# Kernel optimization log

Hardware: AMD Instinct MI355X
Metric: run time of the kernel (lower is better)

Reference implementation:

```python
import jax, jax.numpy as jnp
import numpy as np
import math

B, S, D, H = 4, 2048, 1024, 16
HD = D // H  # head_dim = 64


def _rope_tables(max_len, half_dim, theta=10000.0):
    inv_freq = 1.0 / (theta ** (jnp.arange(0, half_dim, dtype=jnp.float32) / half_dim))
    ang = jnp.arange(max_len, dtype=jnp.float32)[:, None] * inv_freq[None, :]  # [max_len, half_dim]
    return jnp.cos(ang), jnp.sin(ang)


def _apply_rope(x, cos, sin):
    # x: [B, H, S, HD]; cos/sin: [S, HD/2]
    x1, x2 = x[..., ::2], x[..., 1::2]
    # matches torch.cat([x1*cos - x2*sin, x1*sin + x2*cos], dim=-1)
    return jnp.concatenate([x1 * cos - x2 * sin, x1 * sin + x2 * cos], axis=-1)


def setup_inputs() -> dict:
    key = jax.random.key(0)
    kx, kq, ko = jax.random.split(key, 3)
    x = jax.random.normal(kx, (B, S, D), dtype=jnp.float32)
    Wqkv = jax.random.normal(kq, (D, 3 * D), dtype=jnp.float32) / math.sqrt(D)
    Wout = jax.random.normal(ko, (D, D), dtype=jnp.float32) / math.sqrt(D)
    cos, sin = _rope_tables(S, HD // 2)
    # causal additive mask, per-batch as in module signature [B, S, S]
    causal = jnp.where(jnp.tril(jnp.ones((S, S), dtype=bool)), 0.0, -1e9).astype(jnp.float32)
    mask = jnp.broadcast_to(causal, (B, S, S))
    return {"x": x, "cos": cos, "sin": sin, "mask": mask, "Wqkv": Wqkv, "Wout": Wout}


def reference(x, cos, sin, mask, Wqkv, Wout):
    b, s, d = x.shape
    qkv = x @ Wqkv  # [B, S, 3D]
    q, k, v = jnp.split(qkv, 3, axis=-1)
    def to_heads(t):
        return t.reshape(b, s, H, HD).transpose(0, 2, 1, 3)  # [B, H, S, HD]
    q, k, v = to_heads(q), to_heads(k), to_heads(v)
    q = _apply_rope(q, cos[:s], sin[:s])
    k = _apply_rope(k, cos[:s], sin[:s])
    scores = jnp.einsum("bhqd,bhkd->bhqk", q, k) / math.sqrt(HD)
    attn = jax.nn.softmax(scores + mask[:, None, :, :], axis=-1)
    out = jnp.einsum("bhqk,bhkd->bhqd", attn, v)  # [B, H, S, HD]
    out = out.transpose(0, 2, 1, 3).reshape(b, s, d)
    return out @ Wout
```

## Files before the change

### kernel.cpp

```cpp
#include <hip/hip_runtime.h>
#include <hip/hip_bf16.h>
#include <stdint.h>

#define B_   4
#define S_   2048
#define D_   1024
#define H_   16
#define HD_  64
#define BH_  (B_*H_)
#define MROWS (B_*S_)

typedef short  short8  __attribute__((ext_vector_type(8)));
typedef float  floatx4 __attribute__((ext_vector_type(4)));

__device__ __forceinline__ ushort f2bf(float f) {
    union { float f; uint32_t u; } v; v.f = f;
    uint32_t u = v.u;
    return (ushort)((u + 0x7FFFu + ((u >> 16) & 1u)) >> 16);
}
__device__ __forceinline__ float u2f(uint32_t u) {
    union { uint32_t u; float f; } v; v.u = u; return v.f;
}
__device__ __forceinline__ uint32_t f2u(float f) {
    union { float f; uint32_t u; } v; v.f = f; return v.u;
}

__device__ __forceinline__ void gl_lds16(const ushort* g, ushort* l) {
    __builtin_amdgcn_global_load_lds(
        (const __attribute__((address_space(1))) unsigned int*)g,
        (__attribute__((address_space(3))) unsigned int*)l,
        16, 0, 0);
}

__global__ void k_f32_to_bf16(const float* __restrict__ in, ushort* __restrict__ out, int n) {
    int i = (blockIdx.x * blockDim.x + threadIdx.x) * 4;
    if (i + 3 < n) {
        float4 f = *(const float4*)(in + i);
        ushort4 o; o.x = f2bf(f.x); o.y = f2bf(f.y); o.z = f2bf(f.z); o.w = f2bf(f.w);
        *(ushort4*)(out + i) = o;
    }
}

__global__ void k_transpose_to_bf16(const float* __restrict__ in, ushort* __restrict__ out,
                                    int R, int C) {
    __shared__ float tile[32][33];
    int bx = blockIdx.x * 32;
    int by = blockIdx.y * 32;
    int tx = threadIdx.x;
    int ty = threadIdx.y;
    #pragma unroll
    for (int j = 0; j < 32; j += 8)
        tile[ty + j][tx] = in[(size_t)(by + ty + j) * C + bx + tx];
    __syncthreads();
    #pragma unroll
    for (int j = 0; j < 32; j += 8)
        out[(size_t)(bx + ty + j) * R + by + tx] = f2bf(tile[tx][ty + j]);
}

__global__ void k_vtrans(const ushort* __restrict__ Vb, ushort* __restrict__ VbT) {
    __shared__ __align__(16) ushort t[64 * 72];
    int bh = blockIdx.x >> 5;
    int s0 = (blockIdx.x & 31) * 64;
    int tid = threadIdx.x;
    int ss = tid >> 2, c0 = (tid & 3) * 16;
    size_t base = (size_t)bh * S_ * HD_;
    *(uint4*)&t[ss * 72 + c0]     = *(const uint4*)&Vb[base + (size_t)(s0 + ss) * HD_ + c0];
    *(uint4*)&t[ss * 72 + c0 + 8] = *(const uint4*)&Vb[base + (size_t)(s0 + ss) * HD_ + c0 + 8];
    __syncthreads();
    int hd = tid >> 2, q0 = (tid & 3) * 16;
    ushort tmp[16];
    #pragma unroll
    for (int e = 0; e < 16; e++) tmp[e] = t[(q0 + e) * 72 + hd];
    size_t obase = (size_t)bh * HD_ * S_ + (size_t)hd * S_ + s0 + q0;
    *(uint4*)&VbT[obase]     = *(const uint4*)&tmp[0];
    *(uint4*)&VbT[obase + 8] = *(const uint4*)&tmp[8];
}

#define BM 128
#define BN 128
#define BK 64

template<int EPI>
__global__ __launch_bounds__(256)
void k_gemm(const ushort* __restrict__ A, const ushort* __restrict__ Bt,
            float* __restrict__ outF,
            ushort* __restrict__ q_out, ushort* __restrict__ k_out, ushort* __restrict__ v_out,
            int M, int N, int K) {
    __shared__ __align__(16) ushort As[BM * 64];
    __shared__ __align__(16) ushort Bs[BN * 64];
    int tid  = threadIdx.x;
    int lane = tid & 63;
    int wave = tid >> 6;
    int quad = lane >> 4;
    int l16  = lane & 15;
    int bm = blockIdx.y * BM;
    int bn = blockIdx.x * BN;
    int wm = (wave >> 1) * 64;
    int wn = (wave & 1) * 64;

    floatx4 acc[4][4] = {};

    for (int k0 = 0; k0 < K; k0 += BK) {
        __syncthreads();
        #pragma unroll
        for (int i = 0; i < 4; i++) {
            int c   = i * 256 + tid;
            int row = c >> 3;
            int gc  = (c & 7) ^ (row & 7);
            gl_lds16(&A[(size_t)(bm + row) * K + k0 + gc * 8],  &As[c * 8]);
            gl_lds16(&Bt[(size_t)(bn + row) * K + k0 + gc * 8], &Bs[c * 8]);
        }
        __syncthreads();
        #pragma unroll
        for (int kk = 0; kk < 2; kk++) {
            short8 af[4], bf[4];
            #pragma unroll
            for (int mt = 0; mt < 4; mt++)
                af[mt] = *(const short8*)&As[(wm + mt * 16 + l16) * 64 +
                                             (((kk * 4 + quad) ^ (l16 & 7)) << 3)];
            #pragma unroll
            for (int nt = 0; nt < 4; nt++)
                bf[nt] = *(const short8*)&Bs[(wn + nt * 16 + l16) * 64 +
                                             (((kk * 4 + quad) ^ (l16 & 7)) << 3)];
            #pragma unroll
            for (int mt = 0; mt < 4; mt++)
                #pragma unroll
                for (int nt = 0; nt < 4; nt++)
                    acc[mt][nt] = __builtin_amdgcn_mfma_f32_16x16x32_bf16(af[mt], bf[nt], acc[mt][nt], 0, 0, 0);
        }
    }

    #pragma unroll
    for (int mt = 0; mt < 4; mt++)
        #pragma unroll
        for (int nt = 0; nt < 4; nt++)
            #pragma unroll
            for (int r = 0; r < 4; r++) {
                int row = bm + wm + mt * 16 + quad * 4 + r;
                int col = bn + wn + nt * 16 + l16;
                float v = acc[mt][nt][r];
                if (EPI == 0) {
                    int which = col >> 10;
                    int rem   = col & 1023;
                    int h  = rem >> 6, hd = rem & 63;
                    int b  = row >> 11, s  = row & 2047;
                    size_t idx = ((size_t)(b * H_ + h) * S_ + s) * HD_ + hd;
                    ushort bv = f2bf(v);
                    ushort* dst = (which == 0) ? q_out : (which == 1) ? k_out : v_out;
                    dst[idx] = bv;
                } else {
                    outF[(size_t)row * N + col] = v;
                }
            }
}

__global__ void k_rope(ushort* __restrict__ Q, ushort* __restrict__ Kv,
                       const float* __restrict__ cosT, const float* __restrict__ sinT) {
    int wid  = (blockIdx.x * 256 + threadIdx.x) >> 6;
    int lane = threadIdx.x & 63;
    int s  = wid & (S_ - 1);
    int bh = wid >> 11;
    int i  = lane & 31;
    float c  = cosT[s * 32 + i];
    float sn = sinT[s * 32 + i];
    size_t base = ((size_t)bh * S_ + s) * HD_;

    uint32_t uq = *(const uint32_t*)&Q[base + 2 * i];
    float x1 = u2f(uq << 16), x2 = u2f(uq & 0xFFFF0000u);
    float o  = (lane < 32) ? (x1 * c - x2 * sn) : (x1 * sn + x2 * c);
    Q[base + lane] = f2bf(o * 0.1803368801f);

    uint32_t uk = *(const uint32_t*)&Kv[base + 2 * i];
    x1 = u2f(uk << 16); x2 = u2f(uk & 0xFFFF0000u);
    o  = (lane < 32) ? (x1 * c - x2 * sn) : (x1 * sn + x2 * c);
    Kv[base + lane] = f2bf(o);
}

__global__ __launch_bounds__(256, 4)
void k_attn(const ushort* __restrict__ Q, const ushort* __restrict__ K,
            const ushort* __restrict__ VT, ushort* __restrict__ O) {
    __shared__ __align__(16) ushort Ks[64 * 64];
    __shared__ __align__(16) ushort Vt[64 * 64];
    __shared__ __align__(16) ushort Pst[4][32 * 64];

    int tid  = threadIdx.x;
    int lane = tid & 63;
    int wave = tid >> 6;
    int quad = lane >> 4;
    int l16  = lane & 15;

    int bh   = blockIdx.x & 63;
    int qblk = 15 - (blockIdx.x >> 6);
    int qb0  = qblk * 128;
    size_t hbase = (size_t)bh * S_ * HD_;
    size_t vbase = (size_t)bh * HD_ * S_;

    int mrow[2] = { qb0 + wave * 16, qb0 + 64 + wave * 16 };

    short8 qf[2][2];
    #pragma unroll
    for (int m = 0; m < 2; m++)
        #pragma unroll
        for (int h = 0; h < 2; h++)
            qf[m][h] = *(const short8*)&Q[hbase + (size_t)(mrow[m] + l16) * HD_ + quad * 8 + h * 32];

    short8 ones;
    #pragma unroll
    for (int e = 0; e < 8; e++) ones[e] = (short)0x3F80;

    floatx4 acc[2][4] = {};
    floatx4 accl[2] = {};

    int nk = 2 * qblk + 2;
    for (int kb = 0; kb < nk; kb++) {
        int k0 = kb * 64;
        __syncthreads();
        #pragma unroll
        for (int i = 0; i < 2; i++) {
            int c   = i * 256 + tid;
            int row = c >> 3;
            int gc  = (c & 7) ^ (row & 7);
            gl_lds16(&K[hbase + (size_t)(k0 + row) * HD_ + gc * 8], &Ks[c * 8]);
            gl_lds16(&VT[vbase + (size_t)row * S_ + k0 + gc * 8],   &Vt[c * 8]);
        }
        __syncthreads();

        bool act[2] = { k0 <= mrow[0] + 15, k0 <= mrow[1] + 15 };

        #pragma unroll
        for (int m = 0; m < 2; m++) {
            if (!act[m]) continue;
            floatx4 sc[4] = {};
            #pragma unroll
            for (int kt = 0; kt < 4; kt++)
                #pragma unroll
                for (int h = 0; h < 2; h++) {
                    short8 kf = *(const short8*)&Ks[(kt * 16 + l16) * 64 +
                                                    (((h * 4 + quad) ^ (l16 & 7)) << 3)];
                    sc[kt] = __builtin_amdgcn_mfma_f32_16x16x32_bf16(kf, qf[m][h], sc[kt], 0, 0, 0);
                }
            bool needMask = (k0 + 63 > mrow[m]);
            int qr = mrow[m] + l16;
            #pragma unroll
            for (int kt = 0; kt < 4; kt++) {
                float p[4];
                #pragma unroll
                for (int r = 0; r < 4; r++) {
                    float v = exp2f(sc[kt][r]);
                    if (needMask) {
                        int kc = k0 + kt * 16 + quad * 4 + r;
                        if (kc > qr) v = 0.0f;
                    }
                    p[r] = v;
                }
                uint2 pk;
                pk.x = __builtin_amdgcn_perm(f2u(p[1]) + 0x8000u, f2u(p[0]) + 0x8000u, 0x07060302u);
                pk.y = __builtin_amdgcn_perm(f2u(p[3]) + 0x8000u, f2u(p[2]) + 0x8000u, 0x07060302u);
                int pc = (kt * 4 + quad) ^ (l16 & 14);
                *(uint2*)&Pst[wave][(m * 16 + l16) * 64 + pc * 4] = pk;
            }
        }

        #pragma unroll
        for (int k2 = 0; k2 < 2; k2++) {
            short8 vb[4];
            #pragma unroll
            for (int nt = 0; nt < 4; nt++)
                vb[nt] = *(const short8*)&Vt[(nt * 16 + l16) * 64 +
                                             (((k2 * 4 + quad) ^ (l16 & 7)) << 3)];
            #pragma unroll
            for (int m = 0; m < 2; m++) {
                if (!act[m]) continue;
                int pe = (k2 * 8 + quad * 2) ^ (l16 & 14);
                short8 pa = *(const short8*)&Pst[wave][(m * 16 + l16) * 64 + pe * 4];
                #pragma unroll
                for (int nt = 0; nt < 4; nt++)
                    acc[m][nt] = __builtin_amdgcn_mfma_f32_16x16x32_bf16(pa, vb[nt], acc[m][nt], 0, 0, 0);
                accl[m] = __builtin_amdgcn_mfma_f32_16x16x32_bf16(pa, ones, accl[m], 0, 0, 0);
            }
        }
    }

    int b = bh >> 4, h = bh & 15;
    #pragma unroll
    for (int m = 0; m < 2; m++)
        #pragma unroll
        for (int r = 0; r < 4; r++) {
            float inv = 1.0f / accl[m][r];
            int qr = mrow[m] + quad * 4 + r;
            #pragma unroll
            for (int nt = 0; nt < 4; nt++)
                O[((size_t)(b * S_ + qr)) * D_ + h * HD_ + nt * 16 + l16] = f2bf(acc[m][nt][r] * inv);
        }
}

extern "C" void kernel_launch(void* const* d_in, const int* in_sizes, int n_in,
                              void* d_out, int out_size, void* d_ws, size_t ws_size,
                              hipStream_t stream) {
    const float* x    = (const float*)d_in[0];
    const float* cosT = (const float*)d_in[1];
    const float* sinT = (const float*)d_in[2];
    const float* Wqkv = (const float*)d_in[4];
    const float* Wout = (const float*)d_in[5];
    float* out = (float*)d_out;

    ushort* ws = (ushort*)d_ws;
    ushort* Xbf    = ws;
    ushort* WqkvT  = Xbf    + (size_t)MROWS * D_;
    ushort* WoutT  = WqkvT  + (size_t)3 * D_ * D_;
    ushort* Qb     = WoutT  + (size_t)D_ * D_;
    ushort* Kb     = Qb     + (size_t)BH_ * S_ * HD_;
    ushort* Vb     = Kb     + (size_t)BH_ * S_ * HD_;
    ushort* VbT    = Vb     + (size_t)BH_ * S_ * HD_;
    ushort* AO     = Xbf;

    k_f32_to_bf16<<<(MROWS * D_) / 1024, 256, 0, stream>>>(x, Xbf, MROWS * D_);
    k_transpose_to_bf16<<<dim3(3 * D_ / 32, D_ / 32), dim3(32, 8), 0, stream>>>(Wqkv, WqkvT, D_, 3 * D_);
    k_transpose_to_bf16<<<dim3(D_ / 32, D_ / 32), dim3(32, 8), 0, stream>>>(Wout, WoutT, D_, D_);
    k_gemm<0><<<dim3(3 * D_ / BN, MROWS / BM), 256, 0, stream>>>(Xbf, WqkvT, nullptr, Qb, Kb, Vb,
                                                                 MROWS, 3 * D_, D_);
    k_rope<<<(BH_ * S_ * 64) / 256, 256, 0, stream>>>(Qb, Kb, cosT, sinT);
    k_vtrans<<<BH_ * 32, 256, 0, stream>>>(Vb, VbT);
    k_attn<<<1024, 256, 0, stream>>>(Qb, Kb, VbT, AO);
    k_gemm<1><<<dim3(D_ / BN, MROWS / BM), 256, 0, stream>>>(AO, WoutT, out, nullptr, nullptr, nullptr,
                                                             MROWS, D_, D_);
}
```

Measured before the change: 311.3 us.

## Merge prep and rope/vtrans kernels, permute attention block order, hoist load addressing

Combines the x conversion and both weight transposes into a single prep launch, and merges RoPE with the V transpose into one launch, cutting the launch count from eight to five. The attention kernel now takes its query-block order from a fixed permutation table instead of plain descending order, which changes how causal work is spread over CUs. K/V tile load pointers are precomputed once and advanced each iteration, removing per-iteration index arithmetic. The merged kernels carry shared-memory declarations and branches that some paths do not need, which may lower occupancy for the rope part.

```diff
diff --git a/kernel.cpp b/kernel.cpp
--- a/kernel.cpp
+++ b/kernel.cpp
@@ -32,22 +32,24 @@
         16, 0, 0);
 }
 
-__global__ void k_f32_to_bf16(const float* __restrict__ in, ushort* __restrict__ out, int n) {
-    int i = (blockIdx.x * blockDim.x + threadIdx.x) * 4;
-    if (i + 3 < n) {
-        float4 f = *(const float4*)(in + i);
+__global__ __launch_bounds__(256)
+void k_prep(const float* __restrict__ x, const float* __restrict__ Wqkv,
+            const float* __restrict__ Wout,
+            ushort* __restrict__ Xbf, ushort* __restrict__ WqkvT, ushort* __restrict__ WoutT) {
+    __shared__ float tile[32][33];
+    int blk = blockIdx.x;
+    int tid = threadIdx.x;
+    if (blk >= 4096) {
+        int i = (blk - 4096) * 1024 + tid * 4;
+        float4 f = *(const float4*)(x + i);
         ushort4 o; o.x = f2bf(f.x); o.y = f2bf(f.y); o.z = f2bf(f.z); o.w = f2bf(f.w);
-        *(ushort4*)(out + i) = o;
+        *(ushort4*)(Xbf + i) = o;
+        return;
     }
-}
-
-__global__ void k_transpose_to_bf16(const float* __restrict__ in, ushort* __restrict__ out,
-                                    int R, int C) {
-    __shared__ float tile[32][33];
-    int bx = blockIdx.x * 32;
-    int by = blockIdx.y * 32;
-    int tx = threadIdx.x;
-    int ty = threadIdx.y;
+    const float* in; ushort* out; int R, C, bx, by;
+    if (blk < 3072) { in = Wqkv; out = WqkvT; R = D_; C = 3 * D_; bx = (blk % 96) * 32; by = (blk / 96) * 32; }
+    else            { int b2 = blk - 3072; in = Wout; out = WoutT; R = D_; C = D_; bx = (b2 % 32) * 32; by = (b2 / 32) * 32; }
+    int tx = tid & 31, ty = tid >> 5;
     #pragma unroll
     for (int j = 0; j < 32; j += 8)
         tile[ty + j][tx] = in[(size_t)(by + ty + j) * C + bx + tx];
@@ -55,25 +57,6 @@
     #pragma unroll
     for (int j = 0; j < 32; j += 8)
         out[(size_t)(bx + ty + j) * R + by + tx] = f2bf(tile[tx][ty + j]);
-}
-
-__global__ void k_vtrans(const ushort* __restrict__ Vb, ushort* __restrict__ VbT) {
-    __shared__ __align__(16) ushort t[64 * 72];
-    int bh = blockIdx.x >> 5;
-    int s0 = (blockIdx.x & 31) * 64;
-    int tid = threadIdx.x;
-    int ss = tid >> 2, c0 = (tid & 3) * 16;
-    size_t base = (size_t)bh * S_ * HD_;
-    *(uint4*)&t[ss * 72 + c0]     = *(const uint4*)&Vb[base + (size_t)(s0 + ss) * HD_ + c0];
-    *(uint4*)&t[ss * 72 + c0 + 8] = *(const uint4*)&Vb[base + (size_t)(s0 + ss) * HD_ + c0 + 8];
-    __syncthreads();
-    int hd = tid >> 2, q0 = (tid & 3) * 16;
-    ushort tmp[16];
-    #pragma unroll
-    for (int e = 0; e < 16; e++) tmp[e] = t[(q0 + e) * 72 + hd];
-    size_t obase = (size_t)bh * HD_ * S_ + (size_t)hd * S_ + s0 + q0;
-    *(uint4*)&VbT[obase]     = *(const uint4*)&tmp[0];
-    *(uint4*)&VbT[obase + 8] = *(const uint4*)&tmp[8];
 }
 
 #define BM 128
@@ -154,26 +137,49 @@
             }
 }
 
-__global__ void k_rope(ushort* __restrict__ Q, ushort* __restrict__ Kv,
-                       const float* __restrict__ cosT, const float* __restrict__ sinT) {
-    int wid  = (blockIdx.x * 256 + threadIdx.x) >> 6;
-    int lane = threadIdx.x & 63;
-    int s  = wid & (S_ - 1);
-    int bh = wid >> 11;
-    int i  = lane & 31;
-    float c  = cosT[s * 32 + i];
-    float sn = sinT[s * 32 + i];
-    size_t base = ((size_t)bh * S_ + s) * HD_;
-
-    uint32_t uq = *(const uint32_t*)&Q[base + 2 * i];
-    float x1 = u2f(uq << 16), x2 = u2f(uq & 0xFFFF0000u);
-    float o  = (lane < 32) ? (x1 * c - x2 * sn) : (x1 * sn + x2 * c);
-    Q[base + lane] = f2bf(o * 0.1803368801f);
-
-    uint32_t uk = *(const uint32_t*)&Kv[base + 2 * i];
-    x1 = u2f(uk << 16); x2 = u2f(uk & 0xFFFF0000u);
-    o  = (lane < 32) ? (x1 * c - x2 * sn) : (x1 * sn + x2 * c);
-    Kv[base + lane] = f2bf(o);
+__global__ __launch_bounds__(256)
+void k_ropevt(ushort* __restrict__ Q, ushort* __restrict__ Kv,
+              const ushort* __restrict__ Vb, ushort* __restrict__ VbT,
+              const float* __restrict__ cosT, const float* __restrict__ sinT) {
+    __shared__ __align__(16) ushort t[64 * 72];
+    int blk = blockIdx.x;
+    int tid = threadIdx.x;
+    if (blk < 32768) {
+        int wid  = (blk * 256 + tid) >> 6;
+        int lane = tid & 63;
+        int s  = wid & (S_ - 1);
+        int bh = wid >> 11;
+        int i  = lane & 31;
+        float c  = cosT[s * 32 + i];
+        float sn = sinT[s * 32 + i];
+        size_t base = ((size_t)bh * S_ + s) * HD_;
+
+        uint32_t uq = *(const uint32_t*)&Q[base + 2 * i];
+        float x1 = u2f(uq << 16), x2 = u2f(uq & 0xFFFF0000u);
+        float o  = (lane < 32) ? (x1 * c - x2 * sn) : (x1 * sn + x2 * c);
+        Q[base + lane] = f2bf(o * 0.1803368801f);
+
+        uint32_t uk = *(const uint32_t*)&Kv[base + 2 * i];
+        x1 = u2f(uk << 16); x2 = u2f(uk & 0xFFFF0000u);
+        o  = (lane < 32) ? (x1 * c - x2 * sn) : (x1 * sn + x2 * c);
+        Kv[base + lane] = f2bf(o);
+        return;
+    }
+    int b2 = blk - 32768;
+    int bh = b2 >> 5;
+    int s0 = (b2 & 31) * 64;
+    int ss = tid >> 2, c0 = (tid & 3) * 16;
+    size_t base = (size_t)bh * S_ * HD_;
+    *(uint4*)&t[ss * 72 + c0]     = *(const uint4*)&Vb[base + (size_t)(s0 + ss) * HD_ + c0];
+    *(uint4*)&t[ss * 72 + c0 + 8] = *(const uint4*)&Vb[base + (size_t)(s0 + ss) * HD_ + c0 + 8];
+    __syncthreads();
+    int hd = tid >> 2, q0 = (tid & 3) * 16;
+    ushort tmp[16];
+    #pragma unroll
+    for (int e = 0; e < 16; e++) tmp[e] = t[(q0 + e) * 72 + hd];
+    size_t obase = (size_t)bh * HD_ * S_ + (size_t)hd * S_ + s0 + q0;
+    *(uint4*)&VbT[obase]     = *(const uint4*)&tmp[0];
+    *(uint4*)&VbT[obase + 8] = *(const uint4*)&tmp[8];
 }
 
 __global__ __launch_bounds__(256, 4)
@@ -183,6 +189,8 @@
     __shared__ __align__(16) ushort Vt[64 * 64];
     __shared__ __align__(16) ushort Pst[4][32 * 64];
 
+    const int PI[16] = {15,14,11,10, 12,13,8,9, 2,3,6,7, 1,0,5,4};
+
     int tid  = threadIdx.x;
     int lane = tid & 63;
     int wave = tid >> 6;
@@ -190,7 +198,7 @@
     int l16  = lane & 15;
 
     int bh   = blockIdx.x & 63;
-    int qblk = 15 - (blockIdx.x >> 6);
+    int qblk = PI[blockIdx.x >> 6];
     int qb0  = qblk * 128;
     size_t hbase = (size_t)bh * S_ * HD_;
     size_t vbase = (size_t)bh * HD_ * S_;
@@ -210,19 +218,23 @@
 
     floatx4 acc[2][4] = {};
     floatx4 accl[2] = {};
+
+    int c0r = tid >> 3;
+    int c1r = (256 + tid) >> 3;
+    const ushort* kp0 = &K[hbase + (size_t)c0r * HD_ + (((tid & 7) ^ (c0r & 7)) << 3)];
+    const ushort* kp1 = &K[hbase + (size_t)c1r * HD_ + (((tid & 7) ^ (c1r & 7)) << 3)];
+    const ushort* vp0 = &VT[vbase + (size_t)c0r * S_ + (((tid & 7) ^ (c0r & 7)) << 3)];
+    const ushort* vp1 = &VT[vbase + (size_t)c1r * S_ + (((tid & 7) ^ (c1r & 7)) << 3)];
 
     int nk = 2 * qblk + 2;
     for (int kb = 0; kb < nk; kb++) {
         int k0 = kb * 64;
         __syncthreads();
-        #pragma unroll
-        for (int i = 0; i < 2; i++) {
-            int c   = i * 256 + tid;
-            int row = c >> 3;
-            int gc  = (c & 7) ^ (row & 7);
-            gl_lds16(&K[hbase + (size_t)(k0 + row) * HD_ + gc * 8], &Ks[c * 8]);
-            gl_lds16(&VT[vbase + (size_t)row * S_ + k0 + gc * 8],   &Vt[c * 8]);
-        }
+        gl_lds16(kp0, &Ks[tid * 8]);
+        gl_lds16(kp1, &Ks[(256 + tid) * 8]);
+        gl_lds16(vp0, &Vt[tid * 8]);
+        gl_lds16(vp1, &Vt[(256 + tid) * 8]);
+        kp0 += 64 * HD_; kp1 += 64 * HD_; vp0 += 64; vp1 += 64;
         __syncthreads();
 
         bool act[2] = { k0 <= mrow[0] + 15, k0 <= mrow[1] + 15 };
@@ -314,13 +326,10 @@
     ushort* VbT    = Vb     + (size_t)BH_ * S_ * HD_;
     ushort* AO     = Xbf;
 
-    k_f32_to_bf16<<<(MROWS * D_) / 1024, 256, 0, stream>>>(x, Xbf, MROWS * D_);
-    k_transpose_to_bf16<<<dim3(3 * D_ / 32, D_ / 32), dim3(32, 8), 0, stream>>>(Wqkv, WqkvT, D_, 3 * D_);
-    k_transpose_to_bf16<<<dim3(D_ / 32, D_ / 32), dim3(32, 8), 0, stream>>>(Wout, WoutT, D_, D_);
+    k_prep<<<12288, 256, 0, stream>>>(x, Wqkv, Wout, Xbf, WqkvT, WoutT);
     k_gemm<0><<<dim3(3 * D_ / BN, MROWS / BM), 256, 0, stream>>>(Xbf, WqkvT, nullptr, Qb, Kb, Vb,
                                                                  MROWS, 3 * D_, D_);
-    k_rope<<<(BH_ * S_ * 64) / 256, 256, 0, stream>>>(Qb, Kb, cosT, sinT);
-    k_vtrans<<<BH_ * 32, 256, 0, stream>>>(Vb, VbT);
+    k_ropevt<<<34816, 256, 0, stream>>>(Qb, Kb, Vb, VbT, cosT, sinT);
     k_attn<<<1024, 256, 0, stream>>>(Qb, Kb, VbT, AO);
     k_gemm<1><<<dim3(D_ / BN, MROWS / BM), 256, 0, stream>>>(AO, WoutT, out, nullptr, nullptr, nullptr,
                                                              MROWS, D_, D_);
```

New measurement: 307.3 us. About the same (-1.3%).
